# Performance work log

Measured on AMD Instinct MI355X. Metric: run time of the kernel, lower is better.

The kernel has to match this reference:

```python
import math
import jax, jax.numpy as jnp
import numpy as np

# Constants (module-level in original repo; plausible biological values)
LATENCY_EPSILON = 1e-6
HAIR_CELL_COMPRESSION_EXPONENT = 0.3
HAIR_CELL_ADAPTATION_SUPPRESSION = 0.5
AUDITORY_NERVE_ADAPTATION_DECAY = 0.9
AUDITORY_NERVE_ADAPTATION_RATE = 0.1

SAMPLE_RATE = 16000
N_FFT = 512
N_FILTERS = 128
OUTPUT_SIZE = 262144
N_TIMESTEPS = 128
SPARSITY = 0.05
F_MIN, F_MAX = 80.0, 7600.0


def build_filterbank() -> np.ndarray:
    """Mel triangular filterbank, faithful to _create_filterbank (integer bin edges)."""
    hz_to_mel = lambda hz: 2595.0 * math.log10(1.0 + hz / 700.0)
    mel_to_hz = lambda mel: 700.0 * (10.0 ** (mel / 2595.0) - 1.0)
    mel_pts = np.linspace(hz_to_mel(F_MIN), hz_to_mel(F_MAX), N_FILTERS + 2)
    hz_pts = np.array([mel_to_hz(m) for m in mel_pts])
    bins = (hz_pts * N_FFT / SAMPLE_RATE).astype(np.int64)  # .long() truncation
    fb = np.zeros((N_FILTERS, N_FFT // 2 + 1), dtype=np.float32)
    for i in range(N_FILTERS):
        l, c, r = bins[i], bins[i + 1], bins[i + 2]
        for j in range(l, c):
            if c > l:
                fb[i, j] = (j - l) / (c - l)
        for j in range(c, r):
            if r > c:
                fb[i, j] = (r - j) / (r - c)
    return fb


def setup_inputs() -> dict:
    key = jax.random.key(0)
    k_audio, k_w = jax.random.split(key)
    audio = jax.random.normal(k_audio, (SAMPLE_RATE,), dtype=jnp.float32)
    filterbank = jnp.asarray(build_filterbank())  # [n_filters, n_fft//2+1]
    W = jax.random.normal(k_w, (OUTPUT_SIZE, N_FILTERS), dtype=jnp.float32) * 0.02
    b = jnp.zeros((OUTPUT_SIZE,), dtype=jnp.float32)
    adaptation_state = jnp.zeros((N_FILTERS,), dtype=jnp.float32)
    return {"audio": audio, "filterbank": filterbank, "W": W, "b": b,
            "adaptation_state": adaptation_state}


def reference(audio, filterbank, W, b, adaptation_state):
    # Basilar membrane: rfft with n=N_FFT (truncates audio to first N_FFT samples)
    spec = jnp.fft.rfft(audio, n=N_FFT)            # [n_fft//2+1] complex
    magnitude = jnp.abs(spec).astype(jnp.float32)   # [257]
    cochlear = filterbank @ magnitude               # [n_filters]
    # Hair cell compression
    hair = jnp.power(cochlear + LATENCY_EPSILON, HAIR_CELL_COMPRESSION_EXPONENT)
    adapted = jax.nn.relu(hair - adaptation_state * HAIR_CELL_ADAPTATION_SUPPRESSION)
    # Output projection (torch Linear: x @ W.T + b)
    activity = W @ adapted + b                      # [output_size]
    # Latency coding: high activity -> early spike (vectorized scatter)
    a_min, a_max = activity.min(), activity.max()
    norm = (activity - a_min) / (a_max - a_min + 1e-6)
    latencies = ((1.0 - norm) * (N_TIMESTEPS - 1)).astype(jnp.int32)  # [output_size]
    fire = norm > SPARSITY                           # [output_size]
    # spikes[t, n] = fire[n] and latencies[n] == t
    spikes = (latencies[None, :] == jnp.arange(N_TIMESTEPS, dtype=jnp.int32)[:, None]) \
             & fire[None, :]                         # [n_timesteps, output_size] bool
    return spikes
```

## Files before the change

kernel.cpp:

```cpp
#include <hip/hip_runtime.h>
#include <math.h>

#ifndef M_PI
#define M_PI 3.14159265358979323846
#endif

#define N_FFT       512
#define N_BINS      257
#define N_FILTERS   128
#define OUTPUT_SIZE 262144
#define N_TIMESTEPS 128

typedef int int4v __attribute__((ext_vector_type(4)));

__device__ __forceinline__ unsigned long long enc_d(double f) {
    unsigned long long u = (unsigned long long)__double_as_longlong(f);
    return (u & 0x8000000000000000ull) ? ~u : (u | 0x8000000000000000ull);
}
__device__ __forceinline__ double dec_d(unsigned long long e) {
    unsigned long long u = (e & 0x8000000000000000ull) ? (e ^ 0x8000000000000000ull) : ~e;
    return __longlong_as_double((long long)u);
}

__global__ __launch_bounds__(64) void k1a_dft(
    const float* __restrict__ audio, float* __restrict__ mag,
    unsigned long long* __restrict__ minmax)
{
    __shared__ double sre[64];
    __shared__ double sim[64];

    const int b    = blockIdx.x;
    const int lane = threadIdx.x;

    double re = 0.0, im = 0.0;
    #pragma unroll
    for (int j = 0; j < 8; ++j) {
        const int n = lane * 8 + j;
        const int m = (b * n) & (N_FFT - 1);
        double s, c;
        sincos((-2.0 * M_PI * (double)m) / (double)N_FFT, &s, &c);
        const double a = (double)audio[n];
        re += a * c;
        im += a * s;
    }
    sre[lane] = re;
    sim[lane] = im;
    __syncthreads();
    #pragma unroll
    for (int s = 32; s > 0; s >>= 1) {
        if (lane < s) {
            sre[lane] += sre[lane + s];
            sim[lane] += sim[lane + s];
        }
        __syncthreads();
    }
    if (lane == 0) {
        mag[b] = (float)sqrt(sre[0] * sre[0] + sim[0] * sim[0]);
        if (b == 0) {
            minmax[0] = 0xFFFFFFFFFFFFFFFFull;
            minmax[1] = 0ull;
        }
    }
}

__global__ __launch_bounds__(256) void k2_gemv(
    const float4* __restrict__ W4, const float* __restrict__ bias,
    const float* __restrict__ fb, const float* __restrict__ mag,
    const float* __restrict__ adapt, double* __restrict__ activity,
    unsigned long long* __restrict__ minmax)
{
    __shared__ float  magl[N_BINS];
    __shared__ double ad[N_FILTERS];
    __shared__ double red_min[256];
    __shared__ double red_max[256];

    const int tid = threadIdx.x;

    for (int j = tid; j < N_BINS; j += 256) magl[j] = mag[j];
    __syncthreads();

    if (tid < N_FILTERS) {
        const float* row = fb + tid * N_BINS;
        double acc = 0.0;
        int j = 0;
        #pragma unroll 1
        for (int b = 0; b < 8; ++b) {
            float r[32];
            #pragma unroll
            for (int u = 0; u < 32; ++u) r[u] = row[j + u];
            #pragma unroll
            for (int u = 0; u < 32; ++u)
                acc += (double)r[u] * (double)magl[j + u];
            j += 32;
        }
        acc += (double)row[256] * (double)magl[256];
        const double x = acc + 1e-6;
        const double p = pow(x, 0.3);
        const double a = p - (double)adapt[tid] * 0.5;
        ad[tid] = a > 0.0 ? a : 0.0;
    }
    __syncthreads();

    const int gtid = blockIdx.x * 256 + tid;
    const int row  = gtid >> 1;
    const int half = gtid & 1;
    const float4* wrow = W4 + (size_t)row * (N_FILTERS / 4) + half * 16;

    float4 w[16];
    #pragma unroll
    for (int j = 0; j < 16; ++j) w[j] = wrow[j];

    double acc = 0.0;
    #pragma unroll
    for (int j = 0; j < 16; ++j) {
        const int k = half * 64 + j * 4;
        acc += (double)w[j].x * ad[k];
        acc += (double)w[j].y * ad[k + 1];
        acc += (double)w[j].z * ad[k + 2];
        acc += (double)w[j].w * ad[k + 3];
    }

    const double other = __shfl_xor(acc, 1, 64);
    const double lo = half ? other : acc;
    const double hi = half ? acc : other;
    const double a = (lo + hi) + (double)bias[row];
    if (!half) activity[row] = a;

    red_min[tid] = a;
    red_max[tid] = a;
    __syncthreads();
    for (int s = 128; s > 0; s >>= 1) {
        if (tid < s) {
            red_min[tid] = fmin(red_min[tid], red_min[tid + s]);
            red_max[tid] = fmax(red_max[tid], red_max[tid + s]);
        }
        __syncthreads();
    }
    if (tid == 0) {
        atomicMin(&minmax[0], enc_d(red_min[0]));
        atomicMax(&minmax[1], enc_d(red_max[0]));
    }
}

__global__ __launch_bounds__(256) void k3_spikes(
    const double* __restrict__ activity,
    const unsigned long long* __restrict__ minmax,
    int4v* __restrict__ out4)
{
    const int tid = blockIdx.x * 256 + threadIdx.x;
    const double amin = dec_d(minmax[0]);
    const double amax = dec_d(minmax[1]);
    const double denom = (amax - amin) + 1e-6;

    const double nx = (activity[4 * tid + 0] - amin) / denom;
    const double ny = (activity[4 * tid + 1] - amin) / denom;
    const double nz = (activity[4 * tid + 2] - amin) / denom;
    const double nw = (activity[4 * tid + 3] - amin) / denom;

    const int lx = (int)((1.0 - nx) * 127.0);
    const int ly = (int)((1.0 - ny) * 127.0);
    const int lz = (int)((1.0 - nz) * 127.0);
    const int lw = (int)((1.0 - nw) * 127.0);

    const int vx = (nx > 0.05) ? 1 : 0;
    const int vy = (ny > 0.05) ? 1 : 0;
    const int vz = (nz > 0.05) ? 1 : 0;
    const int vw = (nw > 0.05) ? 1 : 0;

    const int t0 = blockIdx.y * (N_TIMESTEPS / 4);
    #pragma unroll 8
    for (int t = t0; t < t0 + N_TIMESTEPS / 4; ++t) {
        int4v v;
        v.x = (lx == t) ? vx : 0;
        v.y = (ly == t) ? vy : 0;
        v.z = (lz == t) ? vz : 0;
        v.w = (lw == t) ? vw : 0;
        out4[(size_t)t * (OUTPUT_SIZE / 4) + tid] = v;
    }
}

extern "C" void kernel_launch(void* const* d_in, const int* in_sizes, int n_in,
                              void* d_out, int out_size, void* d_ws, size_t ws_size,
                              hipStream_t stream) {
    (void)in_sizes; (void)n_in; (void)out_size; (void)ws_size;

    const float* audio = (const float*)d_in[0];
    const float* fb    = (const float*)d_in[1];
    const float* W     = (const float*)d_in[2];
    const float* bias  = (const float*)d_in[3];
    const float* adapt = (const float*)d_in[4];
    int* out = (int*)d_out;

    double* activity = (double*)d_ws;
    unsigned long long* minmax =
        (unsigned long long*)(activity + OUTPUT_SIZE);
    float* mag = (float*)(minmax + 2);

    k1a_dft<<<N_BINS, 64, 0, stream>>>(audio, mag, minmax);
    k2_gemv<<<OUTPUT_SIZE * 2 / 256, 256, 0, stream>>>(
        (const float4*)W, bias, fb, mag, adapt, activity, minmax);
    k3_spikes<<<dim3(OUTPUT_SIZE / 4 / 256, 4), 256, 0, stream>>>(
        activity, minmax, (int4v*)out);
}
```

Measured before the change: 306.8 us.

## Assign four strided W rows per thread in GEMV, cutting blocks fourfold

Each GEMV thread now computes four full output rows spaced 65536 apart, replacing the old scheme of two threads sharing one row and combining via shuffle. The grid shrinks from 2048 to 256 blocks, so the per-block filterbank and hair-cell prologue runs far fewer times in total. The cost is that each thread walks a contiguous 512-byte row, so adjacent lanes read addresses 512 bytes apart and loads are uncoalesced. Fewer blocks also means less parallelism for hiding memory latency.

New measurement: 268.7 us. -12.4%, faster.

```diff
diff --git a/kernel.cpp b/kernel.cpp
--- a/kernel.cpp
+++ b/kernel.cpp
@@ -12,6 +12,7 @@
 #define N_TIMESTEPS 128
 
 typedef int int4v __attribute__((ext_vector_type(4)));
+typedef float f32x4 __attribute__((ext_vector_type(4)));
 
 __device__ __forceinline__ unsigned long long enc_d(double f) {
     unsigned long long u = (unsigned long long)__double_as_longlong(f);
@@ -64,7 +65,7 @@
 }
 
 __global__ __launch_bounds__(256) void k2_gemv(
-    const float4* __restrict__ W4, const float* __restrict__ bias,
+    const f32x4* __restrict__ W4, const float* __restrict__ bias,
     const float* __restrict__ fb, const float* __restrict__ mag,
     const float* __restrict__ adapt, double* __restrict__ activity,
     unsigned long long* __restrict__ minmax)
@@ -101,33 +102,55 @@
     }
     __syncthreads();
 
-    const int gtid = blockIdx.x * 256 + tid;
-    const int row  = gtid >> 1;
-    const int half = gtid & 1;
-    const float4* wrow = W4 + (size_t)row * (N_FILTERS / 4) + half * 16;
-
-    float4 w[16];
-    #pragma unroll
-    for (int j = 0; j < 16; ++j) w[j] = wrow[j];
-
-    double acc = 0.0;
-    #pragma unroll
-    for (int j = 0; j < 16; ++j) {
-        const int k = half * 64 + j * 4;
-        acc += (double)w[j].x * ad[k];
-        acc += (double)w[j].y * ad[k + 1];
-        acc += (double)w[j].z * ad[k + 2];
-        acc += (double)w[j].w * ad[k + 3];
-    }
-
-    const double other = __shfl_xor(acc, 1, 64);
-    const double lo = half ? other : acc;
-    const double hi = half ? acc : other;
-    const double a = (lo + hi) + (double)bias[row];
-    if (!half) activity[row] = a;
-
-    red_min[tid] = a;
-    red_max[tid] = a;
+    const int t = blockIdx.x * 256 + tid;
+    const int r0 = t;
+    const int r1 = t + 65536;
+    const int r2 = t + 131072;
+    const int r3 = t + 196608;
+    const f32x4* p0 = W4 + (size_t)r0 * (N_FILTERS / 4);
+    const f32x4* p1 = W4 + (size_t)r1 * (N_FILTERS / 4);
+    const f32x4* p2 = W4 + (size_t)r2 * (N_FILTERS / 4);
+    const f32x4* p3 = W4 + (size_t)r3 * (N_FILTERS / 4);
+
+    double acc0 = 0.0, acc1 = 0.0, acc2 = 0.0, acc3 = 0.0;
+    #pragma unroll 4
+    for (int j = 0; j < N_FILTERS / 4; ++j) {
+        const f32x4 wa = p0[j];
+        const f32x4 wb = p1[j];
+        const f32x4 wc = p2[j];
+        const f32x4 wd = p3[j];
+        const int k = j * 4;
+        acc0 += (double)wa[0] * ad[k];
+        acc0 += (double)wa[1] * ad[k + 1];
+        acc0 += (double)wa[2] * ad[k + 2];
+        acc0 += (double)wa[3] * ad[k + 3];
+        acc1 += (double)wb[0] * ad[k];
+        acc1 += (double)wb[1] * ad[k + 1];
+        acc1 += (double)wb[2] * ad[k + 2];
+        acc1 += (double)wb[3] * ad[k + 3];
+        acc2 += (double)wc[0] * ad[k];
+        acc2 += (double)wc[1] * ad[k + 1];
+        acc2 += (double)wc[2] * ad[k + 2];
+        acc2 += (double)wc[3] * ad[k + 3];
+        acc3 += (double)wd[0] * ad[k];
+        acc3 += (double)wd[1] * ad[k + 1];
+        acc3 += (double)wd[2] * ad[k + 2];
+        acc3 += (double)wd[3] * ad[k + 3];
+    }
+
+    const double a0 = acc0 + (double)bias[r0];
+    const double a1 = acc1 + (double)bias[r1];
+    const double a2 = acc2 + (double)bias[r2];
+    const double a3 = acc3 + (double)bias[r3];
+    activity[r0] = a0;
+    activity[r1] = a1;
+    activity[r2] = a2;
+    activity[r3] = a3;
+
+    const double mn = fmin(fmin(a0, a1), fmin(a2, a3));
+    const double mx = fmax(fmax(a0, a1), fmax(a2, a3));
+    red_min[tid] = mn;
+    red_max[tid] = mx;
     __syncthreads();
     for (int s = 128; s > 0; s >>= 1) {
         if (tid < s) {
@@ -197,8 +220,8 @@
     float* mag = (float*)(minmax + 2);
 
     k1a_dft<<<N_BINS, 64, 0, stream>>>(audio, mag, minmax);
-    k2_gemv<<<OUTPUT_SIZE * 2 / 256, 256, 0, stream>>>(
-        (const float4*)W, bias, fb, mag, adapt, activity, minmax);
+    k2_gemv<<<OUTPUT_SIZE / 1024, 256, 0, stream>>>(
+        (const f32x4*)W, bias, fb, mag, adapt, activity, minmax);
     k3_spikes<<<dim3(OUTPUT_SIZE / 4 / 256, 4), 256, 0, stream>>>(
         activity, minmax, (int4v*)out);
 }
```

## Restructure GEMV so each wave loops over 128 rows with shuffle reductions

Applied to the files above, without the earlier changes.

The GEMV kernel now runs 512 blocks, and each wavefront handles 128 rows. Each half-wave reads one full W row per iteration as coalesced 16-byte loads and reduces the dot product with xor shuffles. Each thread keeps its four adaptation values in registers and tracks a running min/max, so the prologue (filterbank matvec and pow) and the block reduction run 512 times instead of 2048. The cost is 5 shuffles per row, lower parallelism, and a longer serial loop per wave.

New measurement: 279.1 us. -9.0%, faster.

```diff
diff --git a/kernel.cpp b/kernel.cpp
--- a/kernel.cpp
+++ b/kernel.cpp
@@ -1,5 +1,6 @@
 #include <hip/hip_runtime.h>
 #include <math.h>
+#include <float.h>
 
 #ifndef M_PI
 #define M_PI 3.14159265358979323846
@@ -12,6 +13,7 @@
 #define N_TIMESTEPS 128
 
 typedef int int4v __attribute__((ext_vector_type(4)));
+typedef float f32x4 __attribute__((ext_vector_type(4)));
 
 __device__ __forceinline__ unsigned long long enc_d(double f) {
     unsigned long long u = (unsigned long long)__double_as_longlong(f);
@@ -64,7 +66,7 @@
 }
 
 __global__ __launch_bounds__(256) void k2_gemv(
-    const float4* __restrict__ W4, const float* __restrict__ bias,
+    const f32x4* __restrict__ W4, const float* __restrict__ bias,
     const float* __restrict__ fb, const float* __restrict__ mag,
     const float* __restrict__ adapt, double* __restrict__ activity,
     unsigned long long* __restrict__ minmax)
@@ -101,33 +103,41 @@
     }
     __syncthreads();
 
-    const int gtid = blockIdx.x * 256 + tid;
-    const int row  = gtid >> 1;
-    const int half = gtid & 1;
-    const float4* wrow = W4 + (size_t)row * (N_FILTERS / 4) + half * 16;
-
-    float4 w[16];
-    #pragma unroll
-    for (int j = 0; j < 16; ++j) w[j] = wrow[j];
-
-    double acc = 0.0;
-    #pragma unroll
-    for (int j = 0; j < 16; ++j) {
-        const int k = half * 64 + j * 4;
-        acc += (double)w[j].x * ad[k];
-        acc += (double)w[j].y * ad[k + 1];
-        acc += (double)w[j].z * ad[k + 2];
-        acc += (double)w[j].w * ad[k + 3];
-    }
-
-    const double other = __shfl_xor(acc, 1, 64);
-    const double lo = half ? other : acc;
-    const double hi = half ? acc : other;
-    const double a = (lo + hi) + (double)bias[row];
-    if (!half) activity[row] = a;
-
-    red_min[tid] = a;
-    red_max[tid] = a;
+    const int lane = tid & 63;
+    const int sub  = lane & 31;
+    const int half = lane >> 5;
+    const int wv   = (blockIdx.x * 256 + tid) >> 6;
+
+    const double ad0 = ad[4 * sub];
+    const double ad1 = ad[4 * sub + 1];
+    const double ad2 = ad[4 * sub + 2];
+    const double ad3 = ad[4 * sub + 3];
+
+    const int row0 = wv * 128 + half;
+    const f32x4* wp = W4 + (size_t)row0 * 32 + sub;
+
+    double mn = DBL_MAX, mx = -DBL_MAX;
+    #pragma unroll 4
+    for (int i = 0; i < 64; ++i) {
+        const f32x4 w = wp[(size_t)i * 64];
+        double p = (double)w[0] * ad0;
+        p += (double)w[1] * ad1;
+        p += (double)w[2] * ad2;
+        p += (double)w[3] * ad3;
+        p += __shfl_xor(p, 1, 64);
+        p += __shfl_xor(p, 2, 64);
+        p += __shfl_xor(p, 4, 64);
+        p += __shfl_xor(p, 8, 64);
+        p += __shfl_xor(p, 16, 64);
+        const int r = row0 + 2 * i;
+        const double a = p + (double)bias[r];
+        if (sub == 0) activity[r] = a;
+        mn = fmin(mn, a);
+        mx = fmax(mx, a);
+    }
+
+    red_min[tid] = mn;
+    red_max[tid] = mx;
     __syncthreads();
     for (int s = 128; s > 0; s >>= 1) {
         if (tid < s) {
@@ -197,8 +207,8 @@
     float* mag = (float*)(minmax + 2);
 
     k1a_dft<<<N_BINS, 64, 0, stream>>>(audio, mag, minmax);
-    k2_gemv<<<OUTPUT_SIZE * 2 / 256, 256, 0, stream>>>(
-        (const float4*)W, bias, fb, mag, adapt, activity, minmax);
+    k2_gemv<<<512, 256, 0, stream>>>(
+        (const f32x4*)W, bias, fb, mag, adapt, activity, minmax);
     k3_spikes<<<dim3(OUTPUT_SIZE / 4 / 256, 4), 256, 0, stream>>>(
         activity, minmax, (int4v*)out);
 }
```

## Stage W tile through swizzled LDS with coalesced loads, one row per thread

Applied to the files above, without the earlier changes.

The GEMV now has 128 threads per block, each owning one output row. The block's 128x128 W tile is loaded with fully coalesced float4 reads into a 64KB XOR-swizzled LDS tile, and these loads are issued before the filterbank/compression prologue so they overlap it. This removes the strided per-thread row loads and the cross-lane shuffle. In exchange, the 64KB LDS per block limits occupancy, and every block now computes the 128-filter prologue with all 128 threads.

Measured after the change: 306.4 us. About the same (-0.1%).

```diff
diff --git a/kernel.cpp b/kernel.cpp
--- a/kernel.cpp
+++ b/kernel.cpp
@@ -1,5 +1,6 @@
 #include <hip/hip_runtime.h>
 #include <math.h>
+#include <float.h>
 
 #ifndef M_PI
 #define M_PI 3.14159265358979323846
@@ -12,6 +13,7 @@
 #define N_TIMESTEPS 128
 
 typedef int int4v __attribute__((ext_vector_type(4)));
+typedef float f32x4 __attribute__((ext_vector_type(4)));
 
 __device__ __forceinline__ unsigned long long enc_d(double f) {
     unsigned long long u = (unsigned long long)__double_as_longlong(f);
@@ -63,23 +65,44 @@
     }
 }
 
-__global__ __launch_bounds__(256) void k2_gemv(
-    const float4* __restrict__ W4, const float* __restrict__ bias,
+__global__ __launch_bounds__(128) void k2_gemv(
+    const f32x4* __restrict__ W4, const float* __restrict__ bias,
     const float* __restrict__ fb, const float* __restrict__ mag,
     const float* __restrict__ adapt, double* __restrict__ activity,
     unsigned long long* __restrict__ minmax)
 {
+    __shared__ float  tile[128 * 128];
     __shared__ float  magl[N_BINS];
     __shared__ double ad[N_FILTERS];
-    __shared__ double red_min[256];
-    __shared__ double red_max[256];
+    __shared__ double red_min[128];
+    __shared__ double red_max[128];
 
     const int tid = threadIdx.x;
 
-    for (int j = tid; j < N_BINS; j += 256) magl[j] = mag[j];
-    __syncthreads();
-
-    if (tid < N_FILTERS) {
+    for (int j = tid; j < N_BINS; j += 128) magl[j] = mag[j];
+
+    const f32x4* gsrc = W4 + (size_t)blockIdx.x * 4096;
+    #pragma unroll
+    for (int i = 0; i < 32; i += 4) {
+        const f32x4 v0 = gsrc[(i + 0) * 128 + tid];
+        const f32x4 v1 = gsrc[(i + 1) * 128 + tid];
+        const f32x4 v2 = gsrc[(i + 2) * 128 + tid];
+        const f32x4 v3 = gsrc[(i + 3) * 128 + tid];
+        const int i0 = (i + 0) * 128 + tid;
+        const int i1 = (i + 1) * 128 + tid;
+        const int i2 = (i + 2) * 128 + tid;
+        const int i3 = (i + 3) * 128 + tid;
+        *(f32x4*)((char*)tile + (i0 >> 5) * 512 +
+                  (((i0 & 31) << 4) ^ (((i0 >> 5) & 31) << 4))) = v0;
+        *(f32x4*)((char*)tile + (i1 >> 5) * 512 +
+                  (((i1 & 31) << 4) ^ (((i1 >> 5) & 31) << 4))) = v1;
+        *(f32x4*)((char*)tile + (i2 >> 5) * 512 +
+                  (((i2 & 31) << 4) ^ (((i2 >> 5) & 31) << 4))) = v2;
+        *(f32x4*)((char*)tile + (i3 >> 5) * 512 +
+                  (((i3 & 31) << 4) ^ (((i3 >> 5) & 31) << 4))) = v3;
+    }
+
+    {
         const float* row = fb + tid * N_BINS;
         double acc = 0.0;
         int j = 0;
@@ -101,35 +124,26 @@
     }
     __syncthreads();
 
-    const int gtid = blockIdx.x * 256 + tid;
-    const int row  = gtid >> 1;
-    const int half = gtid & 1;
-    const float4* wrow = W4 + (size_t)row * (N_FILTERS / 4) + half * 16;
-
-    float4 w[16];
-    #pragma unroll
-    for (int j = 0; j < 16; ++j) w[j] = wrow[j];
-
+    const int swz = (tid & 31) << 4;
+    const char* rbase = (const char*)tile + tid * 512;
     double acc = 0.0;
-    #pragma unroll
-    for (int j = 0; j < 16; ++j) {
-        const int k = half * 64 + j * 4;
-        acc += (double)w[j].x * ad[k];
-        acc += (double)w[j].y * ad[k + 1];
-        acc += (double)w[j].z * ad[k + 2];
-        acc += (double)w[j].w * ad[k + 3];
-    }
-
-    const double other = __shfl_xor(acc, 1, 64);
-    const double lo = half ? other : acc;
-    const double hi = half ? acc : other;
-    const double a = (lo + hi) + (double)bias[row];
-    if (!half) activity[row] = a;
+    #pragma unroll 8
+    for (int k4 = 0; k4 < 32; ++k4) {
+        const f32x4 w = *(const f32x4*)(rbase + ((k4 * 16) ^ swz));
+        const int k = k4 * 4;
+        acc += (double)w[0] * ad[k];
+        acc += (double)w[1] * ad[k + 1];
+        acc += (double)w[2] * ad[k + 2];
+        acc += (double)w[3] * ad[k + 3];
+    }
+    const int r = blockIdx.x * 128 + tid;
+    const double a = acc + (double)bias[r];
+    activity[r] = a;
 
     red_min[tid] = a;
     red_max[tid] = a;
     __syncthreads();
-    for (int s = 128; s > 0; s >>= 1) {
+    for (int s = 64; s > 0; s >>= 1) {
         if (tid < s) {
             red_min[tid] = fmin(red_min[tid], red_min[tid + s]);
             red_max[tid] = fmax(red_max[tid], red_max[tid + s]);
@@ -197,8 +211,8 @@
     float* mag = (float*)(minmax + 2);
 
     k1a_dft<<<N_BINS, 64, 0, stream>>>(audio, mag, minmax);
-    k2_gemv<<<OUTPUT_SIZE * 2 / 256, 256, 0, stream>>>(
-        (const float4*)W, bias, fb, mag, adapt, activity, minmax);
+    k2_gemv<<<OUTPUT_SIZE / 128, 128, 0, stream>>>(
+        (const f32x4*)W, bias, fb, mag, adapt, activity, minmax);
     k3_spikes<<<dim3(OUTPUT_SIZE / 4 / 256, 4), 256, 0, stream>>>(
         activity, minmax, (int4v*)out);
 }
```
